# Performance work log

Measured on AMD Instinct MI355X. Metric: run time of the kernel, lower is better.

Reference implementation:

```python
import jax, jax.numpy as jnp
import numpy as np

B = 256
NUM_ROUTES = 1152
NUM_CAPS = 10
D_IN = 8
D_OUT = 16
NUM_ITER = 3
EPS = 1e-5


def setup_inputs() -> dict:
    key = jax.random.key(0)
    k1, k2 = jax.random.split(key)
    u = jax.random.normal(k1, (B, NUM_ROUTES, D_IN), dtype=jnp.float32)
    # learned transform W, torch shape (1, R, C, D_OUT, D_IN) with leading 1 dropped
    W = jax.random.normal(k2, (NUM_ROUTES, NUM_CAPS, D_OUT, D_IN), dtype=jnp.float32)
    return {"u": u, "W": W}


def _squash(x, eps=EPS):
    # In the original, squash sums over the last dim of s_j, which has size 1,
    # so it is effectively elementwise: scale = x^2/(1+x^2), out = scale*x/(|x|+eps)
    sq = x * x
    return sq / (1.0 + sq) * x / (jnp.sqrt(sq) + eps)


def reference(u, W):
    # u_hat[b,r,c,d] = sum_i W[r,c,d,i] * u[b,r,i]   -> (B, R, C, D_OUT)
    u_hat = jnp.einsum('rcdi,bri->brcd', W, u)
    b_ij = jnp.zeros((1, NUM_ROUTES, NUM_CAPS, 1), dtype=u_hat.dtype)
    v = None
    for it in range(NUM_ITER):
        c_ij = jax.nn.softmax(b_ij, axis=1)              # (1, R, C, K), K in {1, D_OUT}
        s = jnp.sum(c_ij * u_hat, axis=1, keepdims=True)  # (B, 1, C, D_OUT)
        v = _squash(s)
        if it < NUM_ITER - 1:
            # a_ij[b,r,c,d] = v[b,0,c,d] * sum_k u_hat[b,r,c,k]  (exact reduction of
            # the original transpose-multiply-sum, avoiding the DxD intermediate)
            a = v * jnp.sum(u_hat, axis=-1, keepdims=True)  # (B, R, C, D_OUT)
            b_ij = b_ij + jnp.mean(a, axis=0, keepdims=True)
    return v.reshape(u.shape[0], NUM_CAPS, D_OUT)
```

## Files before the change

### kernel.cpp

```cpp
#include <hip/hip_runtime.h>
#include <math.h>

#define R_   1152
#define C_   10
#define D_   16
#define I_   8
#define B_   256
#define N_   160
#define K_   9216
#define KS_  32
#define KC_  288

#define OFF_WSUM  0
#define OFF_TT    92160
#define OFF_V     (OFF_TT + 2949120)
#define OFF_BIJ   (OFF_V + 40960)
#define OFF_E     (OFF_BIJ + 184320)
#define OFF_NSA   (OFF_E + 184320)
#define OFF_NSB   (OFF_NSA + 160)
#define OFF_PART  (OFF_NSB + 160)

template <int HASE>
__launch_bounds__(256)
__global__ void gemm_kernel(const float* __restrict__ u, const float* __restrict__ W,
                            const float* __restrict__ E, const float* __restrict__ nsum,
                            float* __restrict__ partials, float* __restrict__ Wsum,
                            float* __restrict__ zA, float* __restrict__ zB) {
    int tid = threadIdx.x;
    if (!HASE && blockIdx.x >= 512) {
        int idx = (blockIdx.x - 512) * 256 + tid;
        int r = idx / (C_ * I_);
        int rem = idx % (C_ * I_);
        int c = rem / I_;
        int i = rem % I_;
        const float* p = W + (size_t)r * (C_ * D_ * I_) + c * (D_ * I_) + i;
        float s = 0.0f;
#pragma unroll
        for (int d = 0; d < D_; ++d) s += p[d * I_];
        Wsum[idx] = s;
        return;
    }

    __shared__ float smem[10240];
    int wave = tid >> 6, lane = tid & 63;
    int ng = lane & 15, bg = lane >> 4;
    int bt = blockIdx.x & 15, ks = blockIdx.x >> 4;
    int b0 = bt * 16;
    int n0 = ng * 10;

    if (!HASE && blockIdx.x == 0 && tid < N_) { zA[tid] = 0.0f; zB[tid] = 0.0f; }

    float acc[4][10];
#pragma unroll
    for (int m = 0; m < 4; ++m)
#pragma unroll
        for (int j = 0; j < 10; ++j) acc[m][j] = 0.0f;

    const float* ur[4];
#pragma unroll
    for (int m = 0; m < 4; ++m) ur[m] = u + (size_t)(b0 + bg * 4 + m) * K_;

    float4 wr[5];
    float  ee[5];
    {
        int r = ks * 36 + wave;
#pragma unroll
        for (int it = 0; it < 5; ++it) {
            int idx = it * 64 + lane;
            wr[it] = *(const float4*)(W + (size_t)r * 1280 + idx * 4);
            if (HASE) {
                int n = idx >> 1;
                ee[it] = E[r * N_ + n] / nsum[n];
            }
        }
    }

    int ldsbase = wave * 1280;
    for (int c = 0; c < 9; ++c) {
#pragma unroll
        for (int it = 0; it < 5; ++it) {
            int idx = it * 64 + lane;
            int n = idx >> 1, ih = (idx & 1) * 4;
            float e = HASE ? ee[it] : 1.0f;
            float* q = &smem[ldsbase + ih * 160 + n];
            q[0]   = wr[it].x * e;
            q[160] = wr[it].y * e;
            q[320] = wr[it].z * e;
            q[480] = wr[it].w * e;
        }
        if (c < 8) {
            int r = ks * 36 + (c + 1) * 4 + wave;
#pragma unroll
            for (int it = 0; it < 5; ++it) {
                int idx = it * 64 + lane;
                wr[it] = *(const float4*)(W + (size_t)r * 1280 + idx * 4);
                if (HASE) {
                    int n = idx >> 1;
                    ee[it] = E[r * N_ + n] / nsum[n];
                }
            }
        }
#pragma unroll
        for (int g = 0; g < 2; ++g) {
            int kabs = ks * KC_ + c * 32 + wave * 8 + g * 4;
            float ua[4][4];
#pragma unroll
            for (int m = 0; m < 4; ++m) {
                float4 tmp = *(const float4*)(ur[m] + kabs);
                ua[m][0] = tmp.x; ua[m][1] = tmp.y; ua[m][2] = tmp.z; ua[m][3] = tmp.w;
            }
#pragma unroll
            for (int t4 = 0; t4 < 4; ++t4) {
                const float* wrow = &smem[ldsbase + (g * 4 + t4) * 160 + n0];
                float w[10];
#pragma unroll
                for (int j = 0; j < 10; j += 2) {
                    float2 ww = *(const float2*)(wrow + j);
                    w[j] = ww.x; w[j + 1] = ww.y;
                }
#pragma unroll
                for (int m = 0; m < 4; ++m)
#pragma unroll
                    for (int j = 0; j < 10; ++j)
                        acc[m][j] = fmaf(ua[m][t4], w[j], acc[m][j]);
            }
        }
    }

    __syncthreads();
#pragma unroll
    for (int m = 0; m < 4; ++m)
#pragma unroll
        for (int j = 0; j < 10; ++j)
            smem[wave * 2560 + (bg * 4 + m) * N_ + n0 + j] = acc[m][j];
    __syncthreads();
    float* outp = partials + (size_t)ks * (B_ * N_) + (size_t)b0 * N_;
    for (int f = tid; f < 2560; f += 256)
        outp[f] = smem[f] + smem[2560 + f] + smem[5120 + f] + smem[7680 + f];
}

template <int DOT>
__global__ void rsv_kernel(const float* __restrict__ partials, float* __restrict__ dst,
                           float scale, const float* __restrict__ u,
                           const float* __restrict__ Wsum, float* __restrict__ tT) {
    int tid = threadIdx.x;
    if (DOT && blockIdx.x >= 160) {
        for (int idx = (blockIdx.x - 160) * 256 + tid; idx < B_ * R_; idx += 360 * 256) {
            int r = idx % R_;
            int b = idx / R_;
            const float4* up = (const float4*)(u + (size_t)idx * I_);
            float4 a0 = up[0], a1 = up[1];
            const float* wp = Wsum + (size_t)r * (C_ * I_);
            float outv[C_];
#pragma unroll
            for (int c = 0; c < C_; ++c) {
                const float4* w4 = (const float4*)(wp + c * I_);
                float4 w0 = w4[0], w1 = w4[1];
                outv[c] = a0.x * w0.x + a0.y * w0.y + a0.z * w0.z + a0.w * w0.w
                        + a1.x * w1.x + a1.y * w1.y + a1.z * w1.z + a1.w * w1.w;
            }
#pragma unroll
            for (int c = 0; c < C_; ++c)
                tT[((size_t)c * B_ + b) * R_ + r] = outv[c];
        }
        return;
    }
    int g = blockIdx.x * 256 + tid;
    float s = 0.0f;
#pragma unroll
    for (int ks = 0; ks < KS_; ++ks) s += partials[(size_t)ks * (B_ * N_) + g];
    s *= scale;
    float sq = s * s;
    dst[g] = sq / (1.0f + sq) * s / (sqrtf(sq) + 1e-5f);
}

__launch_bounds__(256)
__global__ void bupd_kernel(const float* __restrict__ v, const float* __restrict__ tT,
                            float* __restrict__ bij, float* __restrict__ E,
                            float* __restrict__ nsum, int accumulate) {
    __shared__ float vs[B_ * 16];
    __shared__ float red[16 * 256];
    int tid = threadIdx.x;
    int c = blockIdx.x % 10;
    int r0 = (blockIdx.x / 10) * 64;
    int rsub = tid & 63, bs = tid >> 6;

    for (int q = tid; q < 1024; q += 256) {
        int b = q >> 2, d4 = q & 3;
        ((float4*)vs)[q] = *(const float4*)(v + (size_t)b * N_ + c * 16 + d4 * 4);
    }
    __syncthreads();

    float acc[16];
#pragma unroll
    for (int d = 0; d < 16; ++d) acc[d] = 0.0f;

    const float* tp = tT + ((size_t)c * B_ + bs * 64) * R_ + r0 + rsub;
    for (int bb = 0; bb < 64; ++bb) {
        float tv = tp[(size_t)bb * R_];
        const float4* vrow = (const float4*)(vs + (bs * 64 + bb) * 16);
        float4 v0 = vrow[0], v1 = vrow[1], v2 = vrow[2], v3 = vrow[3];
        acc[0]  = fmaf(tv, v0.x, acc[0]);  acc[1]  = fmaf(tv, v0.y, acc[1]);
        acc[2]  = fmaf(tv, v0.z, acc[2]);  acc[3]  = fmaf(tv, v0.w, acc[3]);
        acc[4]  = fmaf(tv, v1.x, acc[4]);  acc[5]  = fmaf(tv, v1.y, acc[5]);
        acc[6]  = fmaf(tv, v1.z, acc[6]);  acc[7]  = fmaf(tv, v1.w, acc[7]);
        acc[8]  = fmaf(tv, v2.x, acc[8]);  acc[9]  = fmaf(tv, v2.y, acc[9]);
        acc[10] = fmaf(tv, v2.z, acc[10]); acc[11] = fmaf(tv, v2.w, acc[11]);
        acc[12] = fmaf(tv, v3.x, acc[12]); acc[13] = fmaf(tv, v3.y, acc[13]);
        acc[14] = fmaf(tv, v3.z, acc[14]); acc[15] = fmaf(tv, v3.w, acc[15]);
    }
#pragma unroll
    for (int d = 0; d < 16; ++d) red[d * 256 + tid] = acc[d];
    __syncthreads();

#pragma unroll
    for (int j = 0; j < 4; ++j) {
        int q = tid + 256 * j;
        int rr = q & 63, d = q >> 6;
        const float* rp = red + d * 256 + rr;
        float s = (rp[0] + rp[64] + rp[128] + rp[192]) * (1.0f / B_);
        int o = (r0 + rr) * N_ + c * 16 + d;
        if (accumulate) s += bij[o];
        bij[o] = s;
        float ex = __expf(s);
        E[o] = ex;
#pragma unroll
        for (int off = 32; off > 0; off >>= 1) ex += __shfl_down(ex, off, 64);
        if (rr == 0) atomicAdd(&nsum[c * 16 + d], ex);
    }
}

extern "C" void kernel_launch(void* const* d_in, const int* in_sizes, int n_in,
                              void* d_out, int out_size, void* d_ws, size_t ws_size,
                              hipStream_t stream) {
    (void)in_sizes; (void)n_in; (void)out_size; (void)ws_size;
    const float* u = (const float*)d_in[0];
    const float* W = (const float*)d_in[1];
    float* out = (float*)d_out;
    float* ws = (float*)d_ws;

    float* Wsum     = ws + OFF_WSUM;
    float* tT       = ws + OFF_TT;
    float* v        = ws + OFF_V;
    float* bij      = ws + OFF_BIJ;
    float* E        = ws + OFF_E;
    float* nsumA    = ws + OFF_NSA;
    float* nsumB    = ws + OFF_NSB;
    float* partials = ws + OFF_PART;

    gemm_kernel<0><<<872, 256, 0, stream>>>(u, W, nullptr, nullptr, partials,
                                            Wsum, nsumA, nsumB);
    rsv_kernel<1><<<520, 256, 0, stream>>>(partials, v, 1.0f / 1152.0f, u, Wsum, tT);
    bupd_kernel<<<180, 256, 0, stream>>>(v, tT, bij, E, nsumA, 0);

    gemm_kernel<1><<<512, 256, 0, stream>>>(u, W, E, nsumA, partials,
                                            nullptr, nullptr, nullptr);
    rsv_kernel<0><<<160, 256, 0, stream>>>(partials, v, 1.0f, nullptr, nullptr, nullptr);
    bupd_kernel<<<180, 256, 0, stream>>>(v, tT, bij, E, nsumB, 1);

    gemm_kernel<1><<<512, 256, 0, stream>>>(u, W, E, nsumB, partials,
                                            nullptr, nullptr, nullptr);
    rsv_kernel<0><<<160, 256, 0, stream>>>(partials, out, 1.0f, nullptr, nullptr, nullptr);
}
```

Baseline: 170.7 us.

## Defer softmax normalization to reduction, prefetch u, and widen bupd grid

```diff
diff --git a/kernel.cpp b/kernel.cpp
--- a/kernel.cpp
+++ b/kernel.cpp
@@ -20,10 +20,14 @@
 #define OFF_NSB   (OFF_NSA + 160)
 #define OFF_PART  (OFF_NSB + 160)
 
+__device__ __forceinline__ float f4c(const float4 v, int i) {
+    return i == 0 ? v.x : i == 1 ? v.y : i == 2 ? v.z : v.w;
+}
+
 template <int HASE>
-__launch_bounds__(256)
+__launch_bounds__(256, 2)
 __global__ void gemm_kernel(const float* __restrict__ u, const float* __restrict__ W,
-                            const float* __restrict__ E, const float* __restrict__ nsum,
+                            const float* __restrict__ E,
                             float* __restrict__ partials, float* __restrict__ Wsum,
                             float* __restrict__ zA, float* __restrict__ zB) {
     int tid = threadIdx.x;
@@ -56,23 +60,24 @@
 #pragma unroll
         for (int j = 0; j < 10; ++j) acc[m][j] = 0.0f;
 
-    const float* ur[4];
-#pragma unroll
-    for (int m = 0; m < 4; ++m) ur[m] = u + (size_t)(b0 + bg * 4 + m) * K_;
+    const float* ubase = u + (size_t)(b0 + bg * 4) * K_ + ks * KC_ + wave * 8;
 
     float4 wr[5];
     float  ee[5];
+    float4 uc[8];
     {
         int r = ks * 36 + wave;
 #pragma unroll
         for (int it = 0; it < 5; ++it) {
             int idx = it * 64 + lane;
             wr[it] = *(const float4*)(W + (size_t)r * 1280 + idx * 4);
-            if (HASE) {
-                int n = idx >> 1;
-                ee[it] = E[r * N_ + n] / nsum[n];
-            }
-        }
+            if (HASE) ee[it] = E[r * N_ + (idx >> 1)];
+        }
+#pragma unroll
+        for (int m = 0; m < 4; ++m)
+#pragma unroll
+            for (int g = 0; g < 2; ++g)
+                uc[m * 2 + g] = *(const float4*)(ubase + (size_t)m * K_ + g * 4);
     }
 
     int ldsbase = wave * 1280;
@@ -88,27 +93,23 @@
             q[320] = wr[it].z * e;
             q[480] = wr[it].w * e;
         }
+        float4 un[8];
         if (c < 8) {
             int r = ks * 36 + (c + 1) * 4 + wave;
 #pragma unroll
             for (int it = 0; it < 5; ++it) {
                 int idx = it * 64 + lane;
                 wr[it] = *(const float4*)(W + (size_t)r * 1280 + idx * 4);
-                if (HASE) {
-                    int n = idx >> 1;
-                    ee[it] = E[r * N_ + n] / nsum[n];
-                }
+                if (HASE) ee[it] = E[r * N_ + (idx >> 1)];
             }
+#pragma unroll
+            for (int m = 0; m < 4; ++m)
+#pragma unroll
+                for (int g = 0; g < 2; ++g)
+                    un[m * 2 + g] = *(const float4*)(ubase + (size_t)m * K_ + (c + 1) * 32 + g * 4);
         }
 #pragma unroll
         for (int g = 0; g < 2; ++g) {
-            int kabs = ks * KC_ + c * 32 + wave * 8 + g * 4;
-            float ua[4][4];
-#pragma unroll
-            for (int m = 0; m < 4; ++m) {
-                float4 tmp = *(const float4*)(ur[m] + kabs);
-                ua[m][0] = tmp.x; ua[m][1] = tmp.y; ua[m][2] = tmp.z; ua[m][3] = tmp.w;
-            }
 #pragma unroll
             for (int t4 = 0; t4 < 4; ++t4) {
                 const float* wrow = &smem[ldsbase + (g * 4 + t4) * 160 + n0];
@@ -119,11 +120,17 @@
                     w[j] = ww.x; w[j + 1] = ww.y;
                 }
 #pragma unroll
-                for (int m = 0; m < 4; ++m)
+                for (int m = 0; m < 4; ++m) {
+                    float uav = f4c(uc[m * 2 + g], t4);
 #pragma unroll
                     for (int j = 0; j < 10; ++j)
-                        acc[m][j] = fmaf(ua[m][t4], w[j], acc[m][j]);
+                        acc[m][j] = fmaf(uav, w[j], acc[m][j]);
+                }
             }
+        }
+        if (c < 8) {
+#pragma unroll
+            for (int q2 = 0; q2 < 8; ++q2) uc[q2] = un[q2];
         }
     }
 
@@ -141,11 +148,12 @@
 
 template <int DOT>
 __global__ void rsv_kernel(const float* __restrict__ partials, float* __restrict__ dst,
-                           float scale, const float* __restrict__ u,
+                           float scale, const float* __restrict__ nsum,
+                           const float* __restrict__ u,
                            const float* __restrict__ Wsum, float* __restrict__ tT) {
     int tid = threadIdx.x;
     if (DOT && blockIdx.x >= 160) {
-        for (int idx = (blockIdx.x - 160) * 256 + tid; idx < B_ * R_; idx += 360 * 256) {
+        for (int idx = (blockIdx.x - 160) * 256 + tid; idx < B_ * R_; idx += 512 * 256) {
             int r = idx % R_;
             int b = idx / R_;
             const float4* up = (const float4*)(u + (size_t)idx * I_);
@@ -169,7 +177,8 @@
     float s = 0.0f;
 #pragma unroll
     for (int ks = 0; ks < KS_; ++ks) s += partials[(size_t)ks * (B_ * N_) + g];
-    s *= scale;
+    if (nsum) s /= nsum[g % N_];
+    else      s *= scale;
     float sq = s * s;
     dst[g] = sq / (1.0f + sq) * s / (sqrtf(sq) + 1e-5f);
 }
@@ -179,11 +188,12 @@
                             float* __restrict__ bij, float* __restrict__ E,
                             float* __restrict__ nsum, int accumulate) {
     __shared__ float vs[B_ * 16];
-    __shared__ float red[16 * 256];
+    __shared__ float red[16 * 258];
+    __shared__ float exs[4][16];
     int tid = threadIdx.x;
     int c = blockIdx.x % 10;
-    int r0 = (blockIdx.x / 10) * 64;
-    int rsub = tid & 63, bs = tid >> 6;
+    int r0 = (blockIdx.x / 10) * 16;
+    int rsub = tid & 15, bs = tid >> 4;
 
     for (int q = tid; q < 1024; q += 256) {
         int b = q >> 2, d4 = q & 3;
@@ -195,10 +205,11 @@
 #pragma unroll
     for (int d = 0; d < 16; ++d) acc[d] = 0.0f;
 
-    const float* tp = tT + ((size_t)c * B_ + bs * 64) * R_ + r0 + rsub;
-    for (int bb = 0; bb < 64; ++bb) {
-        float tv = tp[(size_t)bb * R_];
-        const float4* vrow = (const float4*)(vs + (bs * 64 + bb) * 16);
+    const float* tp = tT + ((size_t)c * B_ + bs) * R_ + r0 + rsub;
+#pragma unroll
+    for (int bb = 0; bb < 16; ++bb) {
+        float tv = tp[(size_t)bb * 16 * R_];
+        const float4* vrow = (const float4*)(vs + (bb * 16 + bs) * 16);
         float4 v0 = vrow[0], v1 = vrow[1], v2 = vrow[2], v3 = vrow[3];
         acc[0]  = fmaf(tv, v0.x, acc[0]);  acc[1]  = fmaf(tv, v0.y, acc[1]);
         acc[2]  = fmaf(tv, v0.z, acc[2]);  acc[3]  = fmaf(tv, v0.w, acc[3]);
@@ -210,24 +221,28 @@
         acc[14] = fmaf(tv, v3.z, acc[14]); acc[15] = fmaf(tv, v3.w, acc[15]);
     }
 #pragma unroll
-    for (int d = 0; d < 16; ++d) red[d * 256 + tid] = acc[d];
-    __syncthreads();
-
-#pragma unroll
-    for (int j = 0; j < 4; ++j) {
-        int q = tid + 256 * j;
-        int rr = q & 63, d = q >> 6;
-        const float* rp = red + d * 256 + rr;
-        float s = (rp[0] + rp[64] + rp[128] + rp[192]) * (1.0f / B_);
-        int o = (r0 + rr) * N_ + c * 16 + d;
-        if (accumulate) s += bij[o];
-        bij[o] = s;
-        float ex = __expf(s);
-        E[o] = ex;
-#pragma unroll
-        for (int off = 32; off > 0; off >>= 1) ex += __shfl_down(ex, off, 64);
-        if (rr == 0) atomicAdd(&nsum[c * 16 + d], ex);
-    }
+    for (int d = 0; d < 16; ++d) red[d * 258 + tid] = acc[d];
+    __syncthreads();
+
+    int d = tid & 15, rr = tid >> 4;
+    const float* rp = red + d * 258 + rr;
+    float s = 0.0f;
+#pragma unroll
+    for (int q = 0; q < 16; ++q) s += rp[q * 16];
+    s *= (1.0f / B_);
+    int o = (r0 + rr) * N_ + c * 16 + d;
+    if (accumulate) s += bij[o];
+    bij[o] = s;
+    float ex = __expf(s);
+    E[o] = ex;
+    ex += __shfl_down(ex, 32, 64);
+    ex += __shfl_down(ex, 16, 64);
+    int wv = tid >> 6, ln = tid & 63;
+    if (ln < 16) exs[wv][ln] = ex;
+    __syncthreads();
+    if (tid < 16)
+        atomicAdd(&nsum[c * 16 + tid],
+                  exs[0][tid] + exs[1][tid] + exs[2][tid] + exs[3][tid]);
 }
 
 extern "C" void kernel_launch(void* const* d_in, const int* in_sizes, int n_in,
@@ -248,17 +263,14 @@
     float* nsumB    = ws + OFF_NSB;
     float* partials = ws + OFF_PART;
 
-    gemm_kernel<0><<<872, 256, 0, stream>>>(u, W, nullptr, nullptr, partials,
-                                            Wsum, nsumA, nsumB);
-    rsv_kernel<1><<<520, 256, 0, stream>>>(partials, v, 1.0f / 1152.0f, u, Wsum, tT);
-    bupd_kernel<<<180, 256, 0, stream>>>(v, tT, bij, E, nsumA, 0);
-
-    gemm_kernel<1><<<512, 256, 0, stream>>>(u, W, E, nsumA, partials,
-                                            nullptr, nullptr, nullptr);
-    rsv_kernel<0><<<160, 256, 0, stream>>>(partials, v, 1.0f, nullptr, nullptr, nullptr);
-    bupd_kernel<<<180, 256, 0, stream>>>(v, tT, bij, E, nsumB, 1);
-
-    gemm_kernel<1><<<512, 256, 0, stream>>>(u, W, E, nsumB, partials,
-                                            nullptr, nullptr, nullptr);
-    rsv_kernel<0><<<160, 256, 0, stream>>>(partials, out, 1.0f, nullptr, nullptr, nullptr);
-}
+    gemm_kernel<0><<<872, 256, 0, stream>>>(u, W, nullptr, partials, Wsum, nsumA, nsumB);
+    rsv_kernel<1><<<672, 256, 0, stream>>>(partials, v, 1.0f / 1152.0f, nullptr, u, Wsum, tT);
+    bupd_kernel<<<720, 256, 0, stream>>>(v, tT, bij, E, nsumA, 0);
+
+    gemm_kernel<1><<<512, 256, 0, stream>>>(u, W, E, partials, nullptr, nullptr, nullptr);
+    rsv_kernel<0><<<160, 256, 0, stream>>>(partials, v, 1.0f, nsumA, nullptr, nullptr, nullptr);
+    bupd_kernel<<<720, 256, 0, stream>>>(v, tT, bij, E, nsumB, 1);
+
+    gemm_kernel<1><<<512, 256, 0, stream>>>(u, W, E, partials, nullptr, nullptr, nullptr);
+    rsv_kernel<0><<<160, 256, 0, stream>>>(partials, out, 1.0f, nsumB, nullptr, nullptr, nullptr);
+}
```

Measured after the change: 143.9 us. 1.19x faster.
